# Performance work log

Measured on AMD Instinct MI355X. Metric: run time of the kernel, lower is better.

Reference implementation:

```python
import jax, jax.numpy as jnp
import numpy as np
from jax import lax

T = 256        # sentence length
V = 50000      # vocab
NT = 50        # POS tags
NL = 40        # dependency labels
WD, TD = 300, 100
IN = WD + TD   # 400, LSTM input & hidden size
H = IN
BI = 2 * H     # 800, biLSTM output per token
MI = 2 * BI    # 1600, MLP input/hidden size


def setup_inputs() -> dict:
    key = jax.random.key(0)
    ks = jax.random.split(key, 32)
    s = 0.05
    d = {
        'words': jax.random.randint(ks[0], (T,), 0, V),
        'tags': jax.random.randint(ks[1], (T,), 0, NT),
        'arcs': jax.random.randint(ks[2], (T + 1,), 0, T + 1),
        'h0': jax.random.normal(ks[3], (4, 1, H), jnp.float32),
        'c0': jax.random.normal(ks[4], (4, 1, H), jnp.float32),
        'word_emb': jax.random.normal(ks[5], (V, WD), jnp.float32) * s,
        'tag_emb': jax.random.normal(ks[6], (NT, TD), jnp.float32) * s,
        # LSTM layer 0: input IN; layer 1: input BI. Leading dim 2 = directions (fwd, rev).
        'Wih0': jax.random.normal(ks[7], (2, 4 * H, IN), jnp.float32) * s,
        'Whh0': jax.random.normal(ks[8], (2, 4 * H, H), jnp.float32) * s,
        'bih0': jax.random.normal(ks[9], (2, 4 * H), jnp.float32) * s,
        'bhh0': jax.random.normal(ks[10], (2, 4 * H), jnp.float32) * s,
        'Wih1': jax.random.normal(ks[11], (2, 4 * H, BI), jnp.float32) * s,
        'Whh1': jax.random.normal(ks[12], (2, 4 * H, H), jnp.float32) * s,
        'bih1': jax.random.normal(ks[13], (2, 4 * H), jnp.float32) * s,
        'bhh1': jax.random.normal(ks[14], (2, 4 * H), jnp.float32) * s,
        # arc-score MLP: 1600 -> 1600 -> 1 (Linear, Tanh, Linear)
        'Wa1': jax.random.normal(ks[15], (MI, MI), jnp.float32) * s,
        'ba1': jax.random.normal(ks[16], (MI,), jnp.float32) * s,
        'Wa2': jax.random.normal(ks[17], (1, MI), jnp.float32) * s,
        'ba2': jax.random.normal(ks[18], (1,), jnp.float32) * s,
        # label MLP: 1600 -> 1600 -> 40
        'Wl1': jax.random.normal(ks[19], (MI, MI), jnp.float32) * s,
        'bl1': jax.random.normal(ks[20], (MI,), jnp.float32) * s,
        'Wl2': jax.random.normal(ks[21], (NL, MI), jnp.float32) * s,
        'bl2': jax.random.normal(ks[22], (NL,), jnp.float32) * s,
    }
    return d


def _lstm_dir(x, Wih, Whh, bih, bhh, h, c):
    # x: [T, in]; returns [T, H]. Torch gate order i, f, g, o.
    xg = x @ Wih.T + (bih + bhh)  # precompute input projection: [T, 4H]

    def step(carry, xt):
        h, c = carry
        g = xt + h @ Whh.T
        i, f, gg, o = jnp.split(g, 4, axis=-1)
        i, f, o = jax.nn.sigmoid(i), jax.nn.sigmoid(f), jax.nn.sigmoid(o)
        c = f * c + i * jnp.tanh(gg)
        h = o * jnp.tanh(c)
        return (h, c), h

    (_, _), ys = lax.scan(step, (h, c), xg)
    return ys


def _bilstm_layer(x, Wih, Whh, bih, bhh, h0f, c0f, h0b, c0b):
    fwd = _lstm_dir(x, Wih[0], Whh[0], bih[0], bhh[0], h0f, c0f)
    bwd = _lstm_dir(x[::-1], Wih[1], Whh[1], bih[1], bhh[1], h0b, c0b)[::-1]
    return jnp.concatenate([fwd, bwd], axis=-1)


def _mlp(z, W1, b1, W2, b2):
    return jnp.tanh(z @ W1.T + b1) @ W2.T + b2


def reference(words, tags, arcs, h0, c0, word_emb, tag_emb,
              Wih0, Whh0, bih0, bhh0, Wih1, Whh1, bih1, bhh1,
              Wa1, ba1, Wa2, ba2, Wl1, bl1, Wl2, bl2):
    n = words.shape[0]
    x = jnp.concatenate([word_emb[words], tag_emb[tags]], axis=-1)  # [T, 400]
    x1 = _bilstm_layer(x, Wih0, Whh0, bih0, bhh0, h0[0, 0], c0[0, 0], h0[1, 0], c0[1, 0])
    hV = _bilstm_layer(x1, Wih1, Whh1, bih1, bhh1, h0[2, 0], c0[2, 0], h0[3, 0], c0[3, 0])  # [T, 800]

    # All-pairs arc scores: feats[h, d] = concat(hV[h], hV[d]) -> MLP -> scalar.
    hh = jnp.broadcast_to(hV[:, None, :], (n, n, BI))
    dd = jnp.broadcast_to(hV[None, :, :], (n, n, BI))
    feats = jnp.concatenate([hh, dd], axis=-1)  # [T, T, 1600]
    raw = _mlp(feats, Wa1, ba1, Wa2, ba2)[..., 0]  # [T, T]
    raw = raw * (1.0 - jnp.eye(n, dtype=raw.dtype))  # head == dep left at 0
    scores = jnp.zeros((n + 1, n + 1), raw.dtype).at[1:, 1:].set(raw).at[0, 0].set(1.0)

    # Labels: for token i with gold head h (1-based), concat(hV[i], hV[h-1]); head==0 -> zeros.
    heads = arcs[1:]
    idx = jnp.clip(heads - 1, 0, n - 1)
    lf = jnp.concatenate([hV, hV[idx]], axis=-1)  # [T, 1600]
    lab = _mlp(lf, Wl1, bl1, Wl2, bl2)  # [T, 40]
    lab = jnp.where((heads == 0)[:, None], jnp.zeros_like(lab), lab)
    return (scores, lab)
```

## Files before the change

### kernel.cpp

```cpp
#include <hip/hip_runtime.h>

typedef unsigned int   u32;
typedef unsigned long long u64;

__device__ __forceinline__ float fast_tanh(float x) {
    x = fminf(fmaxf(x, -15.f), 15.f);
    float e = __expf(2.f * x);
    return __fdividef(e - 1.f, e + 1.f);
}

#define OF_XG   ((size_t)0)
#define OF_H    (OF_XG + 3276800)
#define OF_PQ   (OF_H  + 1638400)
#define OF_U    (OF_PQ + 3276800)

__device__ __forceinline__ float4 hist4(const u64* __restrict__ hist, int t, int k) {
    const u64* p = (k < 400) ? hist + (size_t)t * 400 + k
                             : hist + 102400 + (size_t)(255 - t) * 400 + (k - 400);
    ulonglong2 a = *(const ulonglong2*)p;
    ulonglong2 b = *(const ulonglong2*)(p + 2);
    return make_float4(__uint_as_float((u32)a.x), __uint_as_float((u32)a.y),
                       __uint_as_float((u32)b.x), __uint_as_float((u32)b.y));
}

__global__ __launch_bounds__(256)
void gemm_embed_kernel(const int* __restrict__ words, const int* __restrict__ tags,
                       const float* __restrict__ wemb, const float* __restrict__ temb,
                       const float* __restrict__ B,
                       const float* __restrict__ bias1, const float* __restrict__ bias2,
                       float* __restrict__ C) {
    int t0 = blockIdx.x * 64;
    int n0 = blockIdx.y * 64;
    int tid = threadIdx.x;
    int tx = tid & 15, ty = tid >> 4;
    int lr = tid >> 2, lk = (tid & 3) * 4;
    __shared__ float As[16][68];
    __shared__ float Bs[16][68];
    float acc[4][4] = {};

    int t = t0 + lr;
    const float* arow0 = wemb + (size_t)words[t] * 300;
    const float* arow1 = temb + (size_t)tags[t] * 100 - 300;

    for (int k0 = 0; k0 < 400; k0 += 16) {
        int k = k0 + lk;
        float4 av = (k < 300) ? *(const float4*)(arow0 + k) : *(const float4*)(arow1 + k);
        float4 bv = *(const float4*)(B + (size_t)(n0 + lr) * 400 + k);
        __syncthreads();
        As[lk + 0][lr] = av.x; As[lk + 1][lr] = av.y; As[lk + 2][lr] = av.z; As[lk + 3][lr] = av.w;
        Bs[lk + 0][lr] = bv.x; Bs[lk + 1][lr] = bv.y; Bs[lk + 2][lr] = bv.z; Bs[lk + 3][lr] = bv.w;
        __syncthreads();
        #pragma unroll
        for (int kk = 0; kk < 16; ++kk) {
            float4 a4 = *(const float4*)&As[kk][ty * 4];
            float4 b4 = *(const float4*)&Bs[kk][tx * 4];
            acc[0][0] += a4.x * b4.x; acc[0][1] += a4.x * b4.y; acc[0][2] += a4.x * b4.z; acc[0][3] += a4.x * b4.w;
            acc[1][0] += a4.y * b4.x; acc[1][1] += a4.y * b4.y; acc[1][2] += a4.y * b4.z; acc[1][3] += a4.y * b4.w;
            acc[2][0] += a4.z * b4.x; acc[2][1] += a4.z * b4.y; acc[2][2] += a4.z * b4.z; acc[2][3] += a4.z * b4.w;
            acc[3][0] += a4.w * b4.x; acc[3][1] += a4.w * b4.y; acc[3][2] += a4.w * b4.z; acc[3][3] += a4.w * b4.w;
        }
    }
    float bs[4];
    #pragma unroll
    for (int j = 0; j < 4; ++j) {
        int n = n0 + tx * 4 + j;
        bs[j] = bias1[n] + bias2[n];
    }
    #pragma unroll
    for (int i = 0; i < 4; ++i) {
        int tr = t0 + ty * 4 + i;
        float4 o;
        o.x = acc[i][0] + bs[0]; o.y = acc[i][1] + bs[1];
        o.z = acc[i][2] + bs[2]; o.w = acc[i][3] + bs[3];
        *(float4*)(C + (size_t)tr * 3200 + n0 + tx * 4) = o;
    }
}

__global__ __launch_bounds__(256)
void gemm_hist_kernel(const u64* __restrict__ hist, const int* __restrict__ arcs,
                      const float* __restrict__ B, int ldb, int boff,
                      const float* __restrict__ bias1, const float* __restrict__ bias2,
                      float* __restrict__ C, int ldc, int K, int act) {
    int t0 = blockIdx.x * 64;
    int n0 = blockIdx.y * 64;
    int tid = threadIdx.x;
    int tx = tid & 15, ty = tid >> 4;
    int lr = tid >> 2, lk = (tid & 3) * 4;
    __shared__ float As[16][68];
    __shared__ float Bs[16][68];
    float acc[4][4] = {};

    int t = t0 + lr;
    int tind = t;
    if (arcs) {
        int h = arcs[1 + t];
        tind = min(max(h - 1, 0), 255);
    }

    for (int k0 = 0; k0 < K; k0 += 16) {
        int k = k0 + lk;
        int tt = (k < 800) ? t : tind;
        int kk2 = (k < 800) ? k : k - 800;
        float4 av = hist4(hist, tt, kk2);
        float4 bv = *(const float4*)(B + (size_t)(n0 + lr) * ldb + boff + k0 + lk);
        __syncthreads();
        As[lk + 0][lr] = av.x; As[lk + 1][lr] = av.y; As[lk + 2][lr] = av.z; As[lk + 3][lr] = av.w;
        Bs[lk + 0][lr] = bv.x; Bs[lk + 1][lr] = bv.y; Bs[lk + 2][lr] = bv.z; Bs[lk + 3][lr] = bv.w;
        __syncthreads();
        #pragma unroll
        for (int kk = 0; kk < 16; ++kk) {
            float4 a4 = *(const float4*)&As[kk][ty * 4];
            float4 b4 = *(const float4*)&Bs[kk][tx * 4];
            acc[0][0] += a4.x * b4.x; acc[0][1] += a4.x * b4.y; acc[0][2] += a4.x * b4.z; acc[0][3] += a4.x * b4.w;
            acc[1][0] += a4.y * b4.x; acc[1][1] += a4.y * b4.y; acc[1][2] += a4.y * b4.z; acc[1][3] += a4.y * b4.w;
            acc[2][0] += a4.z * b4.x; acc[2][1] += a4.z * b4.y; acc[2][2] += a4.z * b4.z; acc[2][3] += a4.z * b4.w;
            acc[3][0] += a4.w * b4.x; acc[3][1] += a4.w * b4.y; acc[3][2] += a4.w * b4.z; acc[3][3] += a4.w * b4.w;
        }
    }
    float bs[4];
    #pragma unroll
    for (int j = 0; j < 4; ++j) {
        int n = n0 + tx * 4 + j;
        float b = 0.f;
        if (bias1) b += bias1[n];
        if (bias2) b += bias2[n];
        bs[j] = b;
    }
    #pragma unroll
    for (int i = 0; i < 4; ++i) {
        int tr = t0 + ty * 4 + i;
        float4 o;
        o.x = acc[i][0] + bs[0]; o.y = acc[i][1] + bs[1];
        o.z = acc[i][2] + bs[2]; o.w = acc[i][3] + bs[3];
        if (act) { o.x = fast_tanh(o.x); o.y = fast_tanh(o.y); o.z = fast_tanh(o.z); o.w = fast_tanh(o.w); }
        *(float4*)(C + (size_t)tr * ldc + n0 + tx * 4) = o;
    }
}

__global__ __launch_bounds__(256)
void pq_u_kernel(const u64* __restrict__ hist, const int* __restrict__ arcs,
                 const float* __restrict__ Wa1, const float* __restrict__ ba1,
                 const float* __restrict__ Wl1, const float* __restrict__ bl1,
                 float* __restrict__ PQ, float* __restrict__ U) {
    int t0 = blockIdx.x * 64;
    int by = blockIdx.y;
    int tid = threadIdx.x;
    int tx = tid & 15, ty = tid >> 4;
    int lr = tid >> 2, lk = (tid & 3) * 4;
    __shared__ float As[16][68];
    __shared__ float Bs[16][68];
    float acc[4][4] = {};
    int t = t0 + lr;

    if (by < 25) {
        int n0 = by * 64;
        int h = arcs[1 + t];
        int tind = min(max(h - 1, 0), 255);
        for (int k0 = 0; k0 < 1600; k0 += 16) {
            int k = k0 + lk;
            int tt  = (k < 800) ? t : tind;
            int kk2 = (k < 800) ? k : k - 800;
            float4 av = hist4(hist, tt, kk2);
            float4 bv = *(const float4*)(Wl1 + (size_t)(n0 + lr) * 1600 + k);
            __syncthreads();
            As[lk + 0][lr] = av.x; As[lk + 1][lr] = av.y; As[lk + 2][lr] = av.z; As[lk + 3][lr] = av.w;
            Bs[lk + 0][lr] = bv.x; Bs[lk + 1][lr] = bv.y; Bs[lk + 2][lr] = bv.z; Bs[lk + 3][lr] = bv.w;
            __syncthreads();
            #pragma unroll
            for (int kk = 0; kk < 16; ++kk) {
                float4 a4 = *(const float4*)&As[kk][ty * 4];
                float4 b4 = *(const float4*)&Bs[kk][tx * 4];
                acc[0][0] += a4.x * b4.x; acc[0][1] += a4.x * b4.y; acc[0][2] += a4.x * b4.z; acc[0][3] += a4.x * b4.w;
                acc[1][0] += a4.y * b4.x; acc[1][1] += a4.y * b4.y; acc[1][2] += a4.y * b4.z; acc[1][3] += a4.y * b4.w;
                acc[2][0] += a4.z * b4.x; acc[2][1] += a4.z * b4.y; acc[2][2] += a4.z * b4.z; acc[2][3] += a4.z * b4.w;
                acc[3][0] += a4.w * b4.x; acc[3][1] += a4.w * b4.y; acc[3][2] += a4.w * b4.z; acc[3][3] += a4.w * b4.w;
            }
        }
        float bs[4];
        #pragma unroll
        for (int j = 0; j < 4; ++j) bs[j] = bl1[n0 + tx * 4 + j];
        #pragma unroll
        for (int i = 0; i < 4; ++i) {
            int tr = t0 + ty * 4 + i;
            float4 o;
            o.x = fast_tanh(acc[i][0] + bs[0]); o.y = fast_tanh(acc[i][1] + bs[1]);
            o.z = fast_tanh(acc[i][2] + bs[2]); o.w = fast_tanh(acc[i][3] + bs[3]);
            *(float4*)(U + (size_t)tr * 1600 + n0 + tx * 4) = o;
        }
    } else {
        int n0 = (by - 25) * 64;
        int nn = n0 + lr;
        const float* brow = (nn < 1600) ? Wa1 + (size_t)nn * 1600
                                        : Wa1 + (size_t)(nn - 1600) * 1600 + 800;
        for (int k0 = 0; k0 < 800; k0 += 16) {
            float4 av = hist4(hist, t, k0 + lk);
            float4 bv = *(const float4*)(brow + k0 + lk);
            __syncthreads();
            As[lk + 0][lr] = av.x; As[lk + 1][lr] = av.y; As[lk + 2][lr] = av.z; As[lk + 3][lr] = av.w;
            Bs[lk + 0][lr] = bv.x; Bs[lk + 1][lr] = bv.y; Bs[lk + 2][lr] = bv.z; Bs[lk + 3][lr] = bv.w;
            __syncthreads();
            #pragma unroll
            for (int kk = 0; kk < 16; ++kk) {
                float4 a4 = *(const float4*)&As[kk][ty * 4];
                float4 b4 = *(const float4*)&Bs[kk][tx * 4];
                acc[0][0] += a4.x * b4.x; acc[0][1] += a4.x * b4.y; acc[0][2] += a4.x * b4.z; acc[0][3] += a4.x * b4.w;
                acc[1][0] += a4.y * b4.x; acc[1][1] += a4.y * b4.y; acc[1][2] += a4.y * b4.z; acc[1][3] += a4.y * b4.w;
                acc[2][0] += a4.z * b4.x; acc[2][1] += a4.z * b4.y; acc[2][2] += a4.z * b4.z; acc[2][3] += a4.z * b4.w;
                acc[3][0] += a4.w * b4.x; acc[3][1] += a4.w * b4.y; acc[3][2] += a4.w * b4.z; acc[3][3] += a4.w * b4.w;
            }
        }
        float bs[4];
        #pragma unroll
        for (int j = 0; j < 4; ++j) {
            int n = n0 + tx * 4 + j;
            bs[j] = (n < 1600) ? ba1[n] : 0.f;
        }
        #pragma unroll
        for (int i = 0; i < 4; ++i) {
            int tr = t0 + ty * 4 + i;
            float4 o;
            o.x = acc[i][0] + bs[0]; o.y = acc[i][1] + bs[1];
            o.z = acc[i][2] + bs[2]; o.w = acc[i][3] + bs[3];
            *(float4*)(PQ + (size_t)tr * 3200 + n0 + tx * 4) = o;
        }
    }
}

#define LSTM_G 50
__global__ __launch_bounds__(256)
void lstm_kernel(const float* __restrict__ Whh,
                 const float* __restrict__ h0,
                 const float* __restrict__ c0,
                 int hc_base,
                 const float* __restrict__ xg,
                 u64* __restrict__ hist,
                 u32 tag_base) {
    const int T = 256;
    int bid = blockIdx.x;
    int d  = bid / LSTM_G;
    int wg = bid % LSTM_G;
    int a8 = wg * 8;
    int tid = threadIdx.x;
    int w = tid >> 6, lane = tid & 63;
    int c = lane & 7, r = lane >> 3;
    int gate = r >> 1, jj = r & 1;
    int gr = gate * 400 + a8 + 2 * w + jj;

    __shared__ float hbuf[2][416];

    float4 wv[13];
    const float* wrow = Whh + (size_t)d * 640000 + (size_t)gr * 400;
    #pragma unroll
    for (int i = 0; i < 13; ++i) {
        int k = 4 * (c + 8 * i);
        wv[i] = (k + 3 < 400) ? *(const float4*)(wrow + k) : make_float4(0.f, 0.f, 0.f, 0.f);
    }
    if (tid < 16) { hbuf[0][400 + tid] = 0.f; hbuf[1][400 + tid] = 0.f; }

    float c_state = 0.f;
    if (lane == 0 || lane == 8)
        c_state = c0[(hc_base + d) * 400 + a8 + 2 * w + jj];

    u64* hst = hist + (size_t)d * 102400;
    bool need2 = (tid + 256 < 400);

    for (int t = 0; t < T; ++t) {
        int xt = d ? (T - 1 - t) : t;
        float xgv = xg[(size_t)xt * 3200 + d * 1600 + gr];
        float* hb = hbuf[t & 1];

        if (t == 0) {
            hb[tid] = h0[(hc_base + d) * 400 + tid];
            if (need2) hb[tid + 256] = h0[(hc_base + d) * 400 + tid + 256];
        } else {
            const u64* src = hst + (size_t)(t - 1) * 400;
            u32 want = tag_base + (u32)t;
            bool d1 = false, d2 = !need2;
            while (!(d1 && d2)) {
                u64 v1 = 0, v2 = 0;
                if (!d1) v1 = __hip_atomic_load(&src[tid], __ATOMIC_RELAXED, __HIP_MEMORY_SCOPE_AGENT);
                if (!d2) v2 = __hip_atomic_load(&src[tid + 256], __ATOMIC_RELAXED, __HIP_MEMORY_SCOPE_AGENT);
                if (!d1 && (u32)(v1 >> 32) == want) { hb[tid] = __uint_as_float((u32)v1); d1 = true; }
                if (!d2 && (u32)(v2 >> 32) == want) { hb[tid + 256] = __uint_as_float((u32)v2); d2 = true; }
            }
        }
        __syncthreads();

        const float4* h4 = (const float4*)hb;
        float s = 0.f;
        #pragma unroll
        for (int i = 0; i < 13; ++i) {
            float4 hv = h4[c + 8 * i];
            s += wv[i].x * hv.x + wv[i].y * hv.y + wv[i].z * hv.z + wv[i].w * hv.w;
        }
        s += __shfl_down(s, 4);
        s += __shfl_down(s, 2);
        s += __shfl_down(s, 1);

        float v = 0.f;
        if (c == 0) {
            float tot = s + xgv;
            float arg = (gate == 2) ? 2.f * tot : -tot;
            arg = fminf(fmaxf(arg, -60.f), 60.f);
            float e = __expf(arg);
            v = (gate == 2) ? (e - 1.f) * __frcp_rn(e + 1.f)
                            : __frcp_rn(1.f + e);
        }
        float fv = __shfl(v, lane + 16);
        float gv = __shfl(v, lane + 32);
        float ov = __shfl(v, lane + 48);
        if (lane == 0 || lane == 8) {
            c_state = fv * c_state + v * gv;
            float ec = __expf(fminf(fmaxf(2.f * c_state, -60.f), 60.f));
            float th = (ec - 1.f) * __frcp_rn(ec + 1.f);
            float h = ov * th;
            u64 pk = (((u64)(tag_base + t + 1)) << 32) | (u64)__float_as_uint(h);
            __hip_atomic_store(&hst[(size_t)t * 400 + a8 + 2 * w + jj], pk,
                               __ATOMIC_RELAXED, __HIP_MEMORY_SCOPE_AGENT);
        }
    }
}

__global__ __launch_bounds__(256)
void arc_kernel(const float* __restrict__ PQ,
                const float* __restrict__ Wa2, const float* __restrict__ ba2,
                float* __restrict__ out) {
    int i0 = blockIdx.x * 16, j0 = blockIdx.y * 16;
    int tid = threadIdx.x;
    int ii = tid >> 4, jj = tid & 15;
    __shared__ float Pt[16][65], Qt[16][65];
    __shared__ float W2f[1600];

    if (i0 == 0 && j0 == 0) {
        if (tid < 257) out[tid] = (tid == 0) ? 1.0f : 0.0f;
        out[(size_t)(tid + 1) * 257] = 0.0f;
        if (tid == 0) out[0] = 1.0f;
    }
    for (int m = tid; m < 1600; m += 256) W2f[m] = Wa2[m];
    __syncthreads();

    float acc = 0.f;
    int mm = tid & 63, r4 = tid >> 6;
    for (int m0 = 0; m0 < 1600; m0 += 64) {
        #pragma unroll
        for (int rr = r4; rr < 16; rr += 4) {
            Pt[rr][mm] = PQ[(size_t)(i0 + rr) * 3200 + m0 + mm];
            Qt[rr][mm] = PQ[(size_t)(j0 + rr) * 3200 + 1600 + m0 + mm];
        }
        __syncthreads();
        #pragma unroll 8
        for (int m = 0; m < 64; ++m) {
            float s = Pt[ii][m] + Qt[jj][m];
            acc += W2f[m0 + m] * fast_tanh(s);
        }
        __syncthreads();
    }
    float raw = acc + ba2[0];
    int gi = i0 + ii, gj = j0 + jj;
    if (gi == gj) raw = 0.f;
    out[(size_t)(gi + 1) * 257 + (gj + 1)] = raw;
}

__global__ __launch_bounds__(256)
void label_out_kernel(const float* __restrict__ U, const float* __restrict__ Wl2,
                      const float* __restrict__ bl2, const int* __restrict__ arcs,
                      float* __restrict__ out) {
    int t = blockIdx.x;
    __shared__ float u_l[1600];
    __shared__ float part[4][64];
    for (int m = threadIdx.x; m < 1600; m += 256) u_l[m] = U[(size_t)t * 1600 + m];
    __syncthreads();
    int tid = threadIdx.x;
    int n = tid & 63, p = tid >> 6;
    float acc = 0.f;
    if (n < 40) {
        const float4* wr4 = (const float4*)(Wl2 + (size_t)n * 1600 + p * 400);
        const float*  ub  = u_l + p * 400;
        for (int m = 0; m < 100; ++m) {
            float4 w = wr4[m];
            acc += ub[4*m] * w.x + ub[4*m+1] * w.y + ub[4*m+2] * w.z + ub[4*m+3] * w.w;
        }
    }
    part[p][n] = acc;
    __syncthreads();
    if (tid < 40) {
        float v = part[0][tid] + part[1][tid] + part[2][tid] + part[3][tid] + bl2[tid];
        if (arcs[1 + t] == 0) v = 0.f;
        out[(size_t)t * 40 + tid] = v;
    }
}

extern "C" void kernel_launch(void* const* d_in, const int* in_sizes, int n_in,
                              void* d_out, int out_size, void* d_ws, size_t ws_size,
                              hipStream_t stream) {
    const int*   words = (const int*)d_in[0];
    const int*   tags  = (const int*)d_in[1];
    const int*   arcs  = (const int*)d_in[2];
    const float* h0    = (const float*)d_in[3];
    const float* c0    = (const float*)d_in[4];
    const float* wemb  = (const float*)d_in[5];
    const float* temb  = (const float*)d_in[6];
    const float* Wih0  = (const float*)d_in[7];
    const float* Whh0  = (const float*)d_in[8];
    const float* bih0  = (const float*)d_in[9];
    const float* bhh0  = (const float*)d_in[10];
    const float* Wih1  = (const float*)d_in[11];
    const float* Whh1  = (const float*)d_in[12];
    const float* bih1  = (const float*)d_in[13];
    const float* bhh1  = (const float*)d_in[14];
    const float* Wa1   = (const float*)d_in[15];
    const float* ba1   = (const float*)d_in[16];
    const float* Wa2   = (const float*)d_in[17];
    const float* ba2   = (const float*)d_in[18];
    const float* Wl1   = (const float*)d_in[19];
    const float* bl1   = (const float*)d_in[20];
    const float* Wl2   = (const float*)d_in[21];
    const float* bl2   = (const float*)d_in[22];
    float* out = (float*)d_out;

    char* ws = (char*)d_ws;
    float* xg   = (float*)(ws + OF_XG);
    u64*   hist = (u64*)  (ws + OF_H);
    float* PQ   = (float*)(ws + OF_PQ);
    float* U    = (float*)(ws + OF_U);

    gemm_embed_kernel<<<dim3(4, 50), 256, 0, stream>>>(words, tags, wemb, temb, Wih0, bih0, bhh0, xg);
    lstm_kernel<<<2 * LSTM_G, 256, 0, stream>>>(Whh0, h0, c0, 0, xg, hist, 0u);
    gemm_hist_kernel<<<dim3(4, 50), 256, 0, stream>>>(hist, nullptr, Wih1, 800, 0, bih1, bhh1, xg, 3200, 800, 0);
    lstm_kernel<<<2 * LSTM_G, 256, 0, stream>>>(Whh1, h0, c0, 2, xg, hist, 256u);
    pq_u_kernel<<<dim3(4, 75), 256, 0, stream>>>(hist, arcs, Wa1, ba1, Wl1, bl1, PQ, U);
    arc_kernel<<<dim3(16, 16), 256, 0, stream>>>(PQ, Wa2, ba2, out);
    label_out_kernel<<<256, 256, 0, stream>>>(U, Wl2, bl2, arcs, out + 66049);
}
```

Measured before the change: 1.210 ms.

## Overlap LSTM recurrences with downstream GEMMs via tagged spin-wait consumers

Fuses each LSTM layer with the GEMM that consumes its hidden states into one launch. Extra blocks spin on the tagged history entries the LSTM blocks publish, so the layer-1 input projection and the MLP first layers run while the recurrence is still producing timesteps. Blocks for early timesteps read the forward half first and late ones the reverse half, to follow the order in which values become ready. This removes kernel boundaries and the serial tail of the GEMMs. It relies on all LSTM blocks being co-resident with the spinning blocks, and the spinning consumes CU resources and memory bandwidth that the latency-bound recurrence may need.

Result: slower. 1.265 ms (+4.6%).

```diff
diff --git a/kernel.cpp b/kernel.cpp
--- a/kernel.cpp
+++ b/kernel.cpp
@@ -14,13 +14,42 @@
 #define OF_PQ   (OF_H  + 1638400)
 #define OF_U    (OF_PQ + 3276800)
 
-__device__ __forceinline__ float4 hist4(const u64* __restrict__ hist, int t, int k) {
-    const u64* p = (k < 400) ? hist + (size_t)t * 400 + k
-                             : hist + 102400 + (size_t)(255 - t) * 400 + (k - 400);
-    ulonglong2 a = *(const ulonglong2*)p;
-    ulonglong2 b = *(const ulonglong2*)(p + 2);
-    return make_float4(__uint_as_float((u32)a.x), __uint_as_float((u32)a.y),
-                       __uint_as_float((u32)b.x), __uint_as_float((u32)b.y));
+__device__ __forceinline__ float4 hist4_spin(const u64* __restrict__ hist, int t, int k, u32 base) {
+    const u64* p; u32 want;
+    if (k < 400) { p = hist + (size_t)t * 400 + k;                        want = base + (u32)t + 1u; }
+    else         { p = hist + 102400 + (size_t)(255 - t) * 400 + (k - 400); want = base + (u32)(255 - t) + 1u; }
+    for (;;) {
+        u64 a = __hip_atomic_load(p + 0, __ATOMIC_RELAXED, __HIP_MEMORY_SCOPE_AGENT);
+        u64 b = __hip_atomic_load(p + 1, __ATOMIC_RELAXED, __HIP_MEMORY_SCOPE_AGENT);
+        u64 c = __hip_atomic_load(p + 2, __ATOMIC_RELAXED, __HIP_MEMORY_SCOPE_AGENT);
+        u64 d = __hip_atomic_load(p + 3, __ATOMIC_RELAXED, __HIP_MEMORY_SCOPE_AGENT);
+        if ((u32)(a >> 32) == want && (u32)(b >> 32) == want &&
+            (u32)(c >> 32) == want && (u32)(d >> 32) == want)
+            return make_float4(__uint_as_float((u32)a), __uint_as_float((u32)b),
+                               __uint_as_float((u32)c), __uint_as_float((u32)d));
+        __builtin_amdgcn_s_sleep(32);
+    }
+}
+
+__device__ __forceinline__ void stage16(float (*As)[68], float (*Bs)[68],
+                                        int lk, int lr, float4 av, float4 bv) {
+    __syncthreads();
+    As[lk + 0][lr] = av.x; As[lk + 1][lr] = av.y; As[lk + 2][lr] = av.z; As[lk + 3][lr] = av.w;
+    Bs[lk + 0][lr] = bv.x; Bs[lk + 1][lr] = bv.y; Bs[lk + 2][lr] = bv.z; Bs[lk + 3][lr] = bv.w;
+    __syncthreads();
+}
+
+__device__ __forceinline__ void fma16(float acc[4][4], const float (*As)[68], const float (*Bs)[68],
+                                      int tx, int ty) {
+    #pragma unroll
+    for (int kk = 0; kk < 16; ++kk) {
+        float4 a4 = *(const float4*)&As[kk][ty * 4];
+        float4 b4 = *(const float4*)&Bs[kk][tx * 4];
+        acc[0][0] += a4.x * b4.x; acc[0][1] += a4.x * b4.y; acc[0][2] += a4.x * b4.z; acc[0][3] += a4.x * b4.w;
+        acc[1][0] += a4.y * b4.x; acc[1][1] += a4.y * b4.y; acc[1][2] += a4.y * b4.z; acc[1][3] += a4.y * b4.w;
+        acc[2][0] += a4.z * b4.x; acc[2][1] += a4.z * b4.y; acc[2][2] += a4.z * b4.z; acc[2][3] += a4.z * b4.w;
+        acc[3][0] += a4.w * b4.x; acc[3][1] += a4.w * b4.y; acc[3][2] += a4.w * b4.z; acc[3][3] += a4.w * b4.w;
+    }
 }
 
 __global__ __launch_bounds__(256)
@@ -46,19 +75,8 @@
         int k = k0 + lk;
         float4 av = (k < 300) ? *(const float4*)(arow0 + k) : *(const float4*)(arow1 + k);
         float4 bv = *(const float4*)(B + (size_t)(n0 + lr) * 400 + k);
-        __syncthreads();
-        As[lk + 0][lr] = av.x; As[lk + 1][lr] = av.y; As[lk + 2][lr] = av.z; As[lk + 3][lr] = av.w;
-        Bs[lk + 0][lr] = bv.x; Bs[lk + 1][lr] = bv.y; Bs[lk + 2][lr] = bv.z; Bs[lk + 3][lr] = bv.w;
-        __syncthreads();
-        #pragma unroll
-        for (int kk = 0; kk < 16; ++kk) {
-            float4 a4 = *(const float4*)&As[kk][ty * 4];
-            float4 b4 = *(const float4*)&Bs[kk][tx * 4];
-            acc[0][0] += a4.x * b4.x; acc[0][1] += a4.x * b4.y; acc[0][2] += a4.x * b4.z; acc[0][3] += a4.x * b4.w;
-            acc[1][0] += a4.y * b4.x; acc[1][1] += a4.y * b4.y; acc[1][2] += a4.y * b4.z; acc[1][3] += a4.y * b4.w;
-            acc[2][0] += a4.z * b4.x; acc[2][1] += a4.z * b4.y; acc[2][2] += a4.z * b4.z; acc[2][3] += a4.z * b4.w;
-            acc[3][0] += a4.w * b4.x; acc[3][1] += a4.w * b4.y; acc[3][2] += a4.w * b4.z; acc[3][3] += a4.w * b4.w;
-        }
+        stage16(As, Bs, lk, lr, av, bv);
+        fma16(acc, As, Bs, tx, ty);
     }
     float bs[4];
     #pragma unroll
@@ -76,167 +94,17 @@
     }
 }
 
-__global__ __launch_bounds__(256)
-void gemm_hist_kernel(const u64* __restrict__ hist, const int* __restrict__ arcs,
-                      const float* __restrict__ B, int ldb, int boff,
-                      const float* __restrict__ bias1, const float* __restrict__ bias2,
-                      float* __restrict__ C, int ldc, int K, int act) {
-    int t0 = blockIdx.x * 64;
-    int n0 = blockIdx.y * 64;
-    int tid = threadIdx.x;
-    int tx = tid & 15, ty = tid >> 4;
-    int lr = tid >> 2, lk = (tid & 3) * 4;
-    __shared__ float As[16][68];
-    __shared__ float Bs[16][68];
-    float acc[4][4] = {};
-
-    int t = t0 + lr;
-    int tind = t;
-    if (arcs) {
-        int h = arcs[1 + t];
-        tind = min(max(h - 1, 0), 255);
-    }
-
-    for (int k0 = 0; k0 < K; k0 += 16) {
-        int k = k0 + lk;
-        int tt = (k < 800) ? t : tind;
-        int kk2 = (k < 800) ? k : k - 800;
-        float4 av = hist4(hist, tt, kk2);
-        float4 bv = *(const float4*)(B + (size_t)(n0 + lr) * ldb + boff + k0 + lk);
-        __syncthreads();
-        As[lk + 0][lr] = av.x; As[lk + 1][lr] = av.y; As[lk + 2][lr] = av.z; As[lk + 3][lr] = av.w;
-        Bs[lk + 0][lr] = bv.x; Bs[lk + 1][lr] = bv.y; Bs[lk + 2][lr] = bv.z; Bs[lk + 3][lr] = bv.w;
-        __syncthreads();
-        #pragma unroll
-        for (int kk = 0; kk < 16; ++kk) {
-            float4 a4 = *(const float4*)&As[kk][ty * 4];
-            float4 b4 = *(const float4*)&Bs[kk][tx * 4];
-            acc[0][0] += a4.x * b4.x; acc[0][1] += a4.x * b4.y; acc[0][2] += a4.x * b4.z; acc[0][3] += a4.x * b4.w;
-            acc[1][0] += a4.y * b4.x; acc[1][1] += a4.y * b4.y; acc[1][2] += a4.y * b4.z; acc[1][3] += a4.y * b4.w;
-            acc[2][0] += a4.z * b4.x; acc[2][1] += a4.z * b4.y; acc[2][2] += a4.z * b4.z; acc[2][3] += a4.z * b4.w;
-            acc[3][0] += a4.w * b4.x; acc[3][1] += a4.w * b4.y; acc[3][2] += a4.w * b4.z; acc[3][3] += a4.w * b4.w;
-        }
-    }
-    float bs[4];
-    #pragma unroll
-    for (int j = 0; j < 4; ++j) {
-        int n = n0 + tx * 4 + j;
-        float b = 0.f;
-        if (bias1) b += bias1[n];
-        if (bias2) b += bias2[n];
-        bs[j] = b;
-    }
-    #pragma unroll
-    for (int i = 0; i < 4; ++i) {
-        int tr = t0 + ty * 4 + i;
-        float4 o;
-        o.x = acc[i][0] + bs[0]; o.y = acc[i][1] + bs[1];
-        o.z = acc[i][2] + bs[2]; o.w = acc[i][3] + bs[3];
-        if (act) { o.x = fast_tanh(o.x); o.y = fast_tanh(o.y); o.z = fast_tanh(o.z); o.w = fast_tanh(o.w); }
-        *(float4*)(C + (size_t)tr * ldc + n0 + tx * 4) = o;
-    }
-}
-
-__global__ __launch_bounds__(256)
-void pq_u_kernel(const u64* __restrict__ hist, const int* __restrict__ arcs,
-                 const float* __restrict__ Wa1, const float* __restrict__ ba1,
-                 const float* __restrict__ Wl1, const float* __restrict__ bl1,
-                 float* __restrict__ PQ, float* __restrict__ U) {
-    int t0 = blockIdx.x * 64;
-    int by = blockIdx.y;
-    int tid = threadIdx.x;
-    int tx = tid & 15, ty = tid >> 4;
-    int lr = tid >> 2, lk = (tid & 3) * 4;
-    __shared__ float As[16][68];
-    __shared__ float Bs[16][68];
-    float acc[4][4] = {};
-    int t = t0 + lr;
-
-    if (by < 25) {
-        int n0 = by * 64;
-        int h = arcs[1 + t];
-        int tind = min(max(h - 1, 0), 255);
-        for (int k0 = 0; k0 < 1600; k0 += 16) {
-            int k = k0 + lk;
-            int tt  = (k < 800) ? t : tind;
-            int kk2 = (k < 800) ? k : k - 800;
-            float4 av = hist4(hist, tt, kk2);
-            float4 bv = *(const float4*)(Wl1 + (size_t)(n0 + lr) * 1600 + k);
-            __syncthreads();
-            As[lk + 0][lr] = av.x; As[lk + 1][lr] = av.y; As[lk + 2][lr] = av.z; As[lk + 3][lr] = av.w;
-            Bs[lk + 0][lr] = bv.x; Bs[lk + 1][lr] = bv.y; Bs[lk + 2][lr] = bv.z; Bs[lk + 3][lr] = bv.w;
-            __syncthreads();
-            #pragma unroll
-            for (int kk = 0; kk < 16; ++kk) {
-                float4 a4 = *(const float4*)&As[kk][ty * 4];
-                float4 b4 = *(const float4*)&Bs[kk][tx * 4];
-                acc[0][0] += a4.x * b4.x; acc[0][1] += a4.x * b4.y; acc[0][2] += a4.x * b4.z; acc[0][3] += a4.x * b4.w;
-                acc[1][0] += a4.y * b4.x; acc[1][1] += a4.y * b4.y; acc[1][2] += a4.y * b4.z; acc[1][3] += a4.y * b4.w;
-                acc[2][0] += a4.z * b4.x; acc[2][1] += a4.z * b4.y; acc[2][2] += a4.z * b4.z; acc[2][3] += a4.z * b4.w;
-                acc[3][0] += a4.w * b4.x; acc[3][1] += a4.w * b4.y; acc[3][2] += a4.w * b4.z; acc[3][3] += a4.w * b4.w;
-            }
-        }
-        float bs[4];
-        #pragma unroll
-        for (int j = 0; j < 4; ++j) bs[j] = bl1[n0 + tx * 4 + j];
-        #pragma unroll
-        for (int i = 0; i < 4; ++i) {
-            int tr = t0 + ty * 4 + i;
-            float4 o;
-            o.x = fast_tanh(acc[i][0] + bs[0]); o.y = fast_tanh(acc[i][1] + bs[1]);
-            o.z = fast_tanh(acc[i][2] + bs[2]); o.w = fast_tanh(acc[i][3] + bs[3]);
-            *(float4*)(U + (size_t)tr * 1600 + n0 + tx * 4) = o;
-        }
-    } else {
-        int n0 = (by - 25) * 64;
-        int nn = n0 + lr;
-        const float* brow = (nn < 1600) ? Wa1 + (size_t)nn * 1600
-                                        : Wa1 + (size_t)(nn - 1600) * 1600 + 800;
-        for (int k0 = 0; k0 < 800; k0 += 16) {
-            float4 av = hist4(hist, t, k0 + lk);
-            float4 bv = *(const float4*)(brow + k0 + lk);
-            __syncthreads();
-            As[lk + 0][lr] = av.x; As[lk + 1][lr] = av.y; As[lk + 2][lr] = av.z; As[lk + 3][lr] = av.w;
-            Bs[lk + 0][lr] = bv.x; Bs[lk + 1][lr] = bv.y; Bs[lk + 2][lr] = bv.z; Bs[lk + 3][lr] = bv.w;
-            __syncthreads();
-            #pragma unroll
-            for (int kk = 0; kk < 16; ++kk) {
-                float4 a4 = *(const float4*)&As[kk][ty * 4];
-                float4 b4 = *(const float4*)&Bs[kk][tx * 4];
-                acc[0][0] += a4.x * b4.x; acc[0][1] += a4.x * b4.y; acc[0][2] += a4.x * b4.z; acc[0][3] += a4.x * b4.w;
-                acc[1][0] += a4.y * b4.x; acc[1][1] += a4.y * b4.y; acc[1][2] += a4.y * b4.z; acc[1][3] += a4.y * b4.w;
-                acc[2][0] += a4.z * b4.x; acc[2][1] += a4.z * b4.y; acc[2][2] += a4.z * b4.z; acc[2][3] += a4.z * b4.w;
-                acc[3][0] += a4.w * b4.x; acc[3][1] += a4.w * b4.y; acc[3][2] += a4.w * b4.z; acc[3][3] += a4.w * b4.w;
-            }
-        }
-        float bs[4];
-        #pragma unroll
-        for (int j = 0; j < 4; ++j) {
-            int n = n0 + tx * 4 + j;
-            bs[j] = (n < 1600) ? ba1[n] : 0.f;
-        }
-        #pragma unroll
-        for (int i = 0; i < 4; ++i) {
-            int tr = t0 + ty * 4 + i;
-            float4 o;
-            o.x = acc[i][0] + bs[0]; o.y = acc[i][1] + bs[1];
-            o.z = acc[i][2] + bs[2]; o.w = acc[i][3] + bs[3];
-            *(float4*)(PQ + (size_t)tr * 3200 + n0 + tx * 4) = o;
-        }
-    }
-}
-
 #define LSTM_G 50
-__global__ __launch_bounds__(256)
-void lstm_kernel(const float* __restrict__ Whh,
+__device__ __forceinline__ void lstm_body(int bid,
+                 const float* __restrict__ Whh,
                  const float* __restrict__ h0,
                  const float* __restrict__ c0,
                  int hc_base,
                  const float* __restrict__ xg,
                  u64* __restrict__ hist,
-                 u32 tag_base) {
+                 u32 tag_base,
+                 float (*hbuf)[416]) {
     const int T = 256;
-    int bid = blockIdx.x;
     int d  = bid / LSTM_G;
     int wg = bid % LSTM_G;
     int a8 = wg * 8;
@@ -245,8 +113,6 @@
     int c = lane & 7, r = lane >> 3;
     int gate = r >> 1, jj = r & 1;
     int gr = gate * 400 + a8 + 2 * w + jj;
-
-    __shared__ float hbuf[2][416];
 
     float4 wv[13];
     const float* wrow = Whh + (size_t)d * 640000 + (size_t)gr * 400;
@@ -317,6 +183,139 @@
             u64 pk = (((u64)(tag_base + t + 1)) << 32) | (u64)__float_as_uint(h);
             __hip_atomic_store(&hst[(size_t)t * 400 + a8 + 2 * w + jj], pk,
                                __ATOMIC_RELAXED, __HIP_MEMORY_SCOPE_AGENT);
+        }
+    }
+}
+
+union SmemU {
+    struct { float As[16][68]; float Bs[16][68]; } g;
+    float hbuf[2][416];
+};
+
+__global__ __launch_bounds__(256)
+void lstm0_fused(const float* __restrict__ Whh, const float* __restrict__ h0,
+                 const float* __restrict__ c0, const float* __restrict__ xg0,
+                 u64* __restrict__ hist,
+                 const float* __restrict__ Wih1, const float* __restrict__ bih1,
+                 const float* __restrict__ bhh1, float* __restrict__ xg1) {
+    __shared__ SmemU sm;
+    int bid = blockIdx.x;
+    if (bid < 2 * LSTM_G) {
+        lstm_body(bid, Whh, h0, c0, 0, xg0, hist, 0u, sm.hbuf);
+        return;
+    }
+    int g = bid - 2 * LSTM_G;
+    int t0 = (g & 3) * 64;
+    int n0 = (g >> 2) * 64;
+    int tid = threadIdx.x;
+    int tx = tid & 15, ty = tid >> 4;
+    int lr = tid >> 2, lk = (tid & 3) * 4;
+    float acc[4][4] = {};
+    int t = t0 + lr;
+
+    int first = (t0 >= 128) ? 400 : 0;
+    for (int seg = 0; seg < 2; ++seg) {
+        int kb = first ^ (seg ? 400 : 0);
+        for (int k0 = kb; k0 < kb + 400; k0 += 16) {
+            float4 av = hist4_spin(hist, t, k0 + lk, 0u);
+            float4 bv = *(const float4*)(Wih1 + (size_t)(n0 + lr) * 800 + k0 + lk);
+            stage16(sm.g.As, sm.g.Bs, lk, lr, av, bv);
+            fma16(acc, sm.g.As, sm.g.Bs, tx, ty);
+        }
+    }
+    float bs[4];
+    #pragma unroll
+    for (int j = 0; j < 4; ++j) {
+        int n = n0 + tx * 4 + j;
+        bs[j] = bih1[n] + bhh1[n];
+    }
+    #pragma unroll
+    for (int i = 0; i < 4; ++i) {
+        int tr = t0 + ty * 4 + i;
+        float4 o;
+        o.x = acc[i][0] + bs[0]; o.y = acc[i][1] + bs[1];
+        o.z = acc[i][2] + bs[2]; o.w = acc[i][3] + bs[3];
+        *(float4*)(xg1 + (size_t)tr * 3200 + n0 + tx * 4) = o;
+    }
+}
+
+__global__ __launch_bounds__(256)
+void lstm1_fused(const float* __restrict__ Whh, const float* __restrict__ h0,
+                 const float* __restrict__ c0, const float* __restrict__ xg1,
+                 u64* __restrict__ hist, const int* __restrict__ arcs,
+                 const float* __restrict__ Wa1, const float* __restrict__ ba1,
+                 const float* __restrict__ Wl1, const float* __restrict__ bl1,
+                 float* __restrict__ PQ, float* __restrict__ U) {
+    __shared__ SmemU sm;
+    int bid = blockIdx.x;
+    if (bid < 2 * LSTM_G) {
+        lstm_body(bid, Whh, h0, c0, 2, xg1, hist, 256u, sm.hbuf);
+        return;
+    }
+    int g = bid - 2 * LSTM_G;
+    int t0 = (g & 3) * 64;
+    int by = g >> 2;
+    int tid = threadIdx.x;
+    int tx = tid & 15, ty = tid >> 4;
+    int lr = tid >> 2, lk = (tid & 3) * 4;
+    float acc[4][4] = {};
+    int t = t0 + lr;
+    int first = (t0 >= 128) ? 400 : 0;
+
+    if (by < 25) {
+        int n0 = by * 64;
+        int h = arcs[1 + t];
+        int tind = min(max(h - 1, 0), 255);
+        for (int seg = 0; seg < 3; ++seg) {
+            int kb   = (seg < 2) ? (first ^ (seg ? 400 : 0)) : 800;
+            int klen = (seg < 2) ? 400 : 800;
+            for (int k0 = kb; k0 < kb + klen; k0 += 16) {
+                int k = k0 + lk;
+                float4 av = (k < 800) ? hist4_spin(hist, t, k, 256u)
+                                      : hist4_spin(hist, tind, k - 800, 256u);
+                float4 bv = *(const float4*)(Wl1 + (size_t)(n0 + lr) * 1600 + k);
+                stage16(sm.g.As, sm.g.Bs, lk, lr, av, bv);
+                fma16(acc, sm.g.As, sm.g.Bs, tx, ty);
+            }
+        }
+        float bs[4];
+        #pragma unroll
+        for (int j = 0; j < 4; ++j) bs[j] = bl1[n0 + tx * 4 + j];
+        #pragma unroll
+        for (int i = 0; i < 4; ++i) {
+            int tr = t0 + ty * 4 + i;
+            float4 o;
+            o.x = fast_tanh(acc[i][0] + bs[0]); o.y = fast_tanh(acc[i][1] + bs[1]);
+            o.z = fast_tanh(acc[i][2] + bs[2]); o.w = fast_tanh(acc[i][3] + bs[3]);
+            *(float4*)(U + (size_t)tr * 1600 + n0 + tx * 4) = o;
+        }
+    } else {
+        int n0 = (by - 25) * 64;
+        int nn = n0 + lr;
+        const float* brow = (nn < 1600) ? Wa1 + (size_t)nn * 1600
+                                        : Wa1 + (size_t)(nn - 1600) * 1600 + 800;
+        for (int seg = 0; seg < 2; ++seg) {
+            int kb = first ^ (seg ? 400 : 0);
+            for (int k0 = kb; k0 < kb + 400; k0 += 16) {
+                float4 av = hist4_spin(hist, t, k0 + lk, 256u);
+                float4 bv = *(const float4*)(brow + k0 + lk);
+                stage16(sm.g.As, sm.g.Bs, lk, lr, av, bv);
+                fma16(acc, sm.g.As, sm.g.Bs, tx, ty);
+            }
+        }
+        float bs[4];
+        #pragma unroll
+        for (int j = 0; j < 4; ++j) {
+            int n = n0 + tx * 4 + j;
+            bs[j] = (n < 1600) ? ba1[n] : 0.f;
+        }
+        #pragma unroll
+        for (int i = 0; i < 4; ++i) {
+            int tr = t0 + ty * 4 + i;
+            float4 o;
+            o.x = acc[i][0] + bs[0]; o.y = acc[i][1] + bs[1];
+            o.z = acc[i][2] + bs[2]; o.w = acc[i][3] + bs[3];
+            *(float4*)(PQ + (size_t)tr * 3200 + n0 + tx * 4) = o;
         }
     }
 }
@@ -419,16 +418,15 @@
     float* out = (float*)d_out;
 
     char* ws = (char*)d_ws;
-    float* xg   = (float*)(ws + OF_XG);
+    float* xg0  = (float*)(ws + OF_XG);
     u64*   hist = (u64*)  (ws + OF_H);
-    float* PQ   = (float*)(ws + OF_PQ);
+    float* xg1  = (float*)(ws + OF_PQ);
+    float* PQ   = (float*)(ws + OF_XG);
     float* U    = (float*)(ws + OF_U);
 
-    gemm_embed_kernel<<<dim3(4, 50), 256, 0, stream>>>(words, tags, wemb, temb, Wih0, bih0, bhh0, xg);
-    lstm_kernel<<<2 * LSTM_G, 256, 0, stream>>>(Whh0, h0, c0, 0, xg, hist, 0u);
-    gemm_hist_kernel<<<dim3(4, 50), 256, 0, stream>>>(hist, nullptr, Wih1, 800, 0, bih1, bhh1, xg, 3200, 800, 0);
-    lstm_kernel<<<2 * LSTM_G, 256, 0, stream>>>(Whh1, h0, c0, 2, xg, hist, 256u);
-    pq_u_kernel<<<dim3(4, 75), 256, 0, stream>>>(hist, arcs, Wa1, ba1, Wl1, bl1, PQ, U);
+    gemm_embed_kernel<<<dim3(4, 50), 256, 0, stream>>>(words, tags, wemb, temb, Wih0, bih0, bhh0, xg0);
+    lstm0_fused<<<300, 256, 0, stream>>>(Whh0, h0, c0, xg0, hist, Wih1, bih1, bhh1, xg1);
+    lstm1_fused<<<400, 256, 0, stream>>>(Whh1, h0, c0, xg1, hist, arcs, Wa1, ba1, Wl1, bl1, PQ, U);
     arc_kernel<<<dim3(16, 16), 256, 0, stream>>>(PQ, Wa2, ba2, out);
     label_out_kernel<<<256, 256, 0, stream>>>(U, Wl2, bl2, arcs, out + 66049);
 }
```
